# Performance work log

Hardware: AMD Instinct MI355X
Metric: run time of the kernel (lower is better)

Reference implementation:

```python
import jax, jax.numpy as jnp
import numpy as np

N, F_DIM, T, E, H = 1024, 512, 128, 32768, 512
BETA_1, BETA_T = 1e-4, 0.02
SQRT2 = float(np.sqrt(2.0))


def _layer_norm(z, eps=1e-5):
    mu = z.mean(axis=-1, keepdims=True)
    var = z.var(axis=-1, keepdims=True)
    return (z - mu) / jnp.sqrt(var + eps)


def _schedules():
    # sigmoid beta schedule (get_beta_schedule 'sigmoid')
    betas = 1.0 / (1.0 + np.exp(-np.linspace(-6.0, 6.0, T))) * (BETA_T - BETA_1) + BETA_1
    alphas_bar = np.cumprod(1.0 - betas)
    sqrt_ab = jnp.asarray(np.sqrt(alphas_bar), dtype=jnp.float32)
    sqrt_omab = jnp.asarray(np.sqrt(1.0 - alphas_bar), dtype=jnp.float32)
    return sqrt_ab, sqrt_omab


def setup_inputs() -> dict:
    key = jax.random.key(0)
    k_x, k_n, k_t, k_s, k_d, k_e = jax.random.split(key, 6)
    return {
        "x": jax.random.normal(k_x, (N, F_DIM), dtype=jnp.float32),
        "noise": jax.random.normal(k_n, (N, F_DIM), dtype=jnp.float32),
        "time_emb_table": jax.random.normal(k_e, (T, H), dtype=jnp.float32),
        "src": jax.random.randint(k_s, (E,), 0, N, dtype=jnp.int32),
        "dst": jax.random.randint(k_d, (E,), 0, N, dtype=jnp.int32),
        "t": jax.random.randint(k_t, (N,), 0, T, dtype=jnp.int32),
    }


def reference(x, noise, time_emb_table, src, dst, t):
    sqrt_ab, sqrt_omab = _schedules()
    n = x.shape[0]

    # with torch.no_grad(): x = layer_norm(x)
    x = jax.lax.stop_gradient(_layer_norm(x))

    # build_laplacian: L = diag(rowsum(A/n)) - A/n
    adj = jnp.zeros((n, n), dtype=x.dtype).at[src, dst].set(1.0)
    eps_adj = adj / n
    L = jnp.diag(eps_adj.sum(axis=1)) - eps_adj
    negL = -L

    # precompute_laplacian_diffusion recurrence (faithful to code):
    #   M_t = (-L) @ M_{t-1};  d_t = M_t @ d_{t-1}
    def step(carry, _):
        M, d = carry
        M = negL @ M
        d = M @ d
        return (M, d), d

    _, ds = jax.lax.scan(step, (jnp.eye(n, dtype=x.dtype), x), None, length=T - 1)
    diffused = jnp.concatenate([x[None], ds], axis=0)  # [T, N, F]

    # noise shaping: sqrt(2)*LN(noise), then sign(x)*|noise|
    nz = SQRT2 * _layer_norm(noise)
    nz = jnp.sign(x) * jnp.abs(nz)

    # per-node gather: diffused_x[t[i]][i]
    sel = diffused[t, jnp.arange(n)]  # [N, F]

    x_t = sqrt_ab[t][:, None] * sel + sqrt_omab[t][:, None] * nz
    time_embed = time_emb_table[t]  # [N, H]
    return x_t, time_embed
```

## Files before the change

### kernel.cpp

```cpp
#include <hip/hip_runtime.h>

#define NN 1024
#define FD 512
#define TT 128
#define EE 32768

__global__ __launch_bounds__(256) void k_fused(const float* __restrict__ x,
                                               const float* __restrict__ noise,
                                               const float* __restrict__ table,
                                               const int* __restrict__ src,
                                               const int* __restrict__ dst,
                                               const int* __restrict__ t,
                                               float* __restrict__ out) {
    __shared__ float red[4][4];
    __shared__ double dpart[2];
    __shared__ unsigned int bits[32];
    __shared__ int sn[NN];
    __shared__ int nsh;
    __shared__ float acc[4][FD];

    const int i = blockIdx.x;
    const int tid = threadIdx.x;
    const int wv = tid >> 6, ln = tid & 63;
    const int ti = t[i];

    float2 xv = ((const float2*)x)[i * 256 + tid];
    float2 nv = ((const float2*)noise)[i * 256 + tid];
    float sx = xv.x + xv.y, sxx = xv.x * xv.x + xv.y * xv.y;
    float sw = nv.x + nv.y, sww = nv.x * nv.x + nv.y * nv.y;
#pragma unroll
    for (int off = 32; off > 0; off >>= 1) {
        sx  += __shfl_down(sx, off);
        sxx += __shfl_down(sxx, off);
        sw  += __shfl_down(sw, off);
        sww += __shfl_down(sww, off);
    }

    double term = 0.0;
    if (tid <= ti) {
        double xk = -6.0 + 12.0 * (double)tid / 127.0;
        double beta = 1.0 / (1.0 + exp(-xk)) * (0.02 - 1e-4) + 1e-4;
        term = log1p(-beta);
    }
#pragma unroll
    for (int off = 1; off < 64; off <<= 1) term += __shfl_xor(term, off);

    if (ln == 0) { red[0][wv] = sx; red[1][wv] = sxx; red[2][wv] = sw; red[3][wv] = sww; }
    if (ln == 0 && wv < 2) dpart[wv] = term;
    __syncthreads();
    sx  = red[0][0] + red[0][1] + red[0][2] + red[0][3];
    sxx = red[1][0] + red[1][1] + red[1][2] + red[1][3];
    sw  = red[2][0] + red[2][1] + red[2][2] + red[2][3];
    sww = red[3][0] + red[3][1] + red[3][2] + red[3][3];
    const float inv = 1.0f / FD;
    float mux = sx * inv, varx = sxx * inv - mux * mux;
    float rsx = rsqrtf(varx + 1e-5f);
    float mun = sw * inv, varn = sww * inv - mun * mun;
    float rsn = rsqrtf(varn + 1e-5f);
    const float SQ2 = 1.41421356237309515f;
    float2 p; p.x = (xv.x - mux) * rsx; p.y = (xv.y - mux) * rsx;
    float a0n = fabsf((nv.x - mun) * rsn) * SQ2;
    float a1n = fabsf((nv.y - mun) * rsn) * SQ2;
    float s0 = (p.x > 0.f) ? 1.f : ((p.x < 0.f) ? -1.f : 0.f);
    float s1 = (p.y > 0.f) ? 1.f : ((p.y < 0.f) ? -1.f : 0.f);
    float2 z; z.x = s0 * a0n; z.y = s1 * a1n;

    double S = dpart[0] + dpart[1];
    float sa = (float)sqrt(exp(S));
    float so = (float)sqrt(-expm1(S));

    float2 sel = make_float2(0.f, 0.f);
    if (ti == 0) {
        sel = p;
    } else if (ti == 1) {
        if (tid < 32) bits[tid] = 0u;
        if (tid == 0) nsh = 0;
        for (int f = tid; f < FD; f += 256) {
            acc[0][f] = 0.f; acc[1][f] = 0.f; acc[2][f] = 0.f; acc[3][f] = 0.f;
        }
        __syncthreads();
        const int4* s4 = (const int4*)src;
        const int4* d4 = (const int4*)dst;
        for (int q = tid; q < EE / 4; q += 256) {
            int4 sv = s4[q];
            if ((sv.x == i) | (sv.y == i) | (sv.z == i) | (sv.w == i)) {
                int4 dv = d4[q];
                if (sv.x == i) atomicOr(&bits[((unsigned)dv.x) >> 5], 1u << (dv.x & 31));
                if (sv.y == i) atomicOr(&bits[((unsigned)dv.y) >> 5], 1u << (dv.y & 31));
                if (sv.z == i) atomicOr(&bits[((unsigned)dv.z) >> 5], 1u << (dv.z & 31));
                if (sv.w == i) atomicOr(&bits[((unsigned)dv.w) >> 5], 1u << (dv.w & 31));
            }
        }
        __syncthreads();
        if (tid < 32) {
            unsigned int m = bits[tid];
            while (m) {
                int b = __ffs(m) - 1;
                m &= m - 1;
                sn[atomicAdd(&nsh, 1)] = tid * 32 + b;
            }
        }
        __syncthreads();
        int d = nsh;
        for (int k = wv; k < d; k += 4) {
            int j = sn[k];
            const float* xr = x + (size_t)j * FD;
            float v[8];
#pragma unroll
            for (int c = 0; c < 8; c++) v[c] = xr[ln + 64 * c];
            float s = 0.f, ss = 0.f;
#pragma unroll
            for (int c = 0; c < 8; c++) { s += v[c]; ss += v[c] * v[c]; }
#pragma unroll
            for (int off = 1; off < 64; off <<= 1) {
                s  += __shfl_xor(s, off);
                ss += __shfl_xor(ss, off);
            }
            float mu = s * inv;
            float rs = rsqrtf(ss * inv - mu * mu + 1e-5f);
#pragma unroll
            for (int c = 0; c < 8; c++) acc[wv][ln + 64 * c] += (v[c] - mu) * rs;
        }
        __syncthreads();
        float b0 = acc[0][2 * tid]     + acc[1][2 * tid]     + acc[2][2 * tid]     + acc[3][2 * tid];
        float b1 = acc[0][2 * tid + 1] + acc[1][2 * tid + 1] + acc[2][2 * tid + 1] + acc[3][2 * tid + 1];
        const float inv_n = 1.0f / NN;
        sel.x = (b0 - (float)d * p.x) * inv_n;
        sel.y = (b1 - (float)d * p.y) * inv_n;
    }

    float2 o; o.x = sa * sel.x + so * z.x; o.y = sa * sel.y + so * z.y;
    ((float2*)out)[(size_t)i * 256 + tid] = o;
    ((float2*)out)[(size_t)(NN + i) * 256 + tid] =
        ((const float2*)(table + (size_t)ti * FD))[tid];
}

extern "C" void kernel_launch(void* const* d_in, const int* in_sizes, int n_in,
                              void* d_out, int out_size, void* d_ws, size_t ws_size,
                              hipStream_t stream) {
    const float* x     = (const float*)d_in[0];
    const float* noise = (const float*)d_in[1];
    const float* table = (const float*)d_in[2];
    const int*   src   = (const int*)d_in[3];
    const int*   dst   = (const int*)d_in[4];
    const int*   t     = (const int*)d_in[5];
    float* out = (float*)d_out;
    (void)d_ws; (void)ws_size; (void)in_sizes; (void)n_in;

    k_fused<<<NN, 256, 0, stream>>>(x, noise, table, src, dst, t, out);
}
```

Baseline: 88.74 us.

## Prefilter edges whose source has t==1 in a separate compaction kernel

Adds a pre-pass kernel that scans all edges once and compacts only those whose source node has timestep 1 into per-segment lists in workspace, packing src and dst into a single int. The main kernel's t==1 blocks then read these short lists instead of each scanning the full 128 KB src array. This is meant to cut redundant global edge scans across blocks, at the cost of an extra kernel launch and a workspace dependency.

```diff
diff --git a/kernel.cpp b/kernel.cpp
--- a/kernel.cpp
+++ b/kernel.cpp
@@ -4,14 +4,36 @@
 #define FD 512
 #define TT 128
 #define EE 32768
+#define NSEG 128
 
-__global__ __launch_bounds__(256) void k_fused(const float* __restrict__ x,
-                                               const float* __restrict__ noise,
-                                               const float* __restrict__ table,
-                                               const int* __restrict__ src,
-                                               const int* __restrict__ dst,
-                                               const int* __restrict__ t,
-                                               float* __restrict__ out) {
+#define OFF_CNTS 0
+#define OFF_LIST 4096
+
+__global__ __launch_bounds__(256) void k_filter(const int* __restrict__ src,
+                                                const int* __restrict__ dst,
+                                                const int* __restrict__ t,
+                                                int* __restrict__ list,
+                                                int* __restrict__ cnts) {
+    __shared__ int c;
+    if (threadIdx.x == 0) c = 0;
+    __syncthreads();
+    int e = blockIdx.x * 256 + threadIdx.x;
+    int s = src[e];
+    if (t[s] == 1) {
+        int d = dst[e];
+        list[blockIdx.x * 256 + atomicAdd(&c, 1)] = (s << 10) | d;
+    }
+    __syncthreads();
+    if (threadIdx.x == 0) cnts[blockIdx.x] = c;
+}
+
+__global__ __launch_bounds__(256) void k_main(const float* __restrict__ x,
+                                              const float* __restrict__ noise,
+                                              const float* __restrict__ table,
+                                              const int* __restrict__ t,
+                                              const int* __restrict__ list,
+                                              const int* __restrict__ cnts,
+                                              float* __restrict__ out) {
     __shared__ float red[4][4];
     __shared__ double dpart[2];
     __shared__ unsigned int bits[32];
@@ -79,16 +101,12 @@
             acc[0][f] = 0.f; acc[1][f] = 0.f; acc[2][f] = 0.f; acc[3][f] = 0.f;
         }
         __syncthreads();
-        const int4* s4 = (const int4*)src;
-        const int4* d4 = (const int4*)dst;
-        for (int q = tid; q < EE / 4; q += 256) {
-            int4 sv = s4[q];
-            if ((sv.x == i) | (sv.y == i) | (sv.z == i) | (sv.w == i)) {
-                int4 dv = d4[q];
-                if (sv.x == i) atomicOr(&bits[((unsigned)dv.x) >> 5], 1u << (dv.x & 31));
-                if (sv.y == i) atomicOr(&bits[((unsigned)dv.y) >> 5], 1u << (dv.y & 31));
-                if (sv.z == i) atomicOr(&bits[((unsigned)dv.z) >> 5], 1u << (dv.z & 31));
-                if (sv.w == i) atomicOr(&bits[((unsigned)dv.w) >> 5], 1u << (dv.w & 31));
+        for (int b = wv; b < NSEG; b += 4) {
+            int c = cnts[b];
+            for (int k = ln; k < c; k += 64) {
+                int pk = list[b * 256 + k];
+                if ((pk >> 10) == i)
+                    atomicOr(&bits[(pk & 1023) >> 5], 1u << (pk & 31));
             }
         }
         __syncthreads();
@@ -145,7 +163,11 @@
     const int*   dst   = (const int*)d_in[4];
     const int*   t     = (const int*)d_in[5];
     float* out = (float*)d_out;
-    (void)d_ws; (void)ws_size; (void)in_sizes; (void)n_in;
 
-    k_fused<<<NN, 256, 0, stream>>>(x, noise, table, src, dst, t, out);
+    char* w = (char*)d_ws;
+    int* cnts = (int*)(w + OFF_CNTS);
+    int* list = (int*)(w + OFF_LIST);
+
+    k_filter<<<NSEG, 256, 0, stream>>>(src, dst, t, list, cnts);
+    k_main<<<NN, 256, 0, stream>>>(x, noise, table, t, list, cnts, out);
 }
```

Result: slower. 91.68 us (+3.3%).
